# Performance work log

Hardware: AMD Instinct MI355X
Metric: run time of the kernel (lower is better)

Reference implementation:

```python
import jax, jax.numpy as jnp
import numpy as np

N = 100000
IN_F = 165
HID = 128
E = 1600000


def gcn_conv(x, W, b, src, dst, n):
    # PyG GCNConv: h = x @ W; add self-loops; symmetric norm D^-1/2 A D^-1/2; aggregate; + bias
    h = x @ W  # [n, out]
    src_sl = jnp.concatenate([src, jnp.arange(n)])
    dst_sl = jnp.concatenate([dst, jnp.arange(n)])
    deg = jax.ops.segment_sum(jnp.ones_like(src_sl, dtype=h.dtype), dst_sl, num_segments=n)
    dinv = jnp.where(deg > 0, jax.lax.rsqrt(deg), 0.0)
    norm = dinv[src_sl] * dinv[dst_sl]  # [e+n]
    msg = h[src_sl] * norm[:, None]
    out = jax.ops.segment_sum(msg, dst_sl, num_segments=n)
    return out + b


def setup_inputs() -> dict:
    key = jax.random.key(0)
    k = jax.random.split(key, 8)
    x = jax.random.normal(k[0], (N, IN_F), dtype=jnp.float32)
    edge_index = jax.random.randint(k[1], (2, E), 0, N)
    s1 = 1.0 / np.sqrt(IN_F)
    s2 = 1.0 / np.sqrt(HID)
    W1 = jax.random.uniform(k[2], (IN_F, HID), jnp.float32, -s1, s1)
    b1 = jnp.zeros((HID,), jnp.float32)
    W2 = jax.random.uniform(k[3], (HID, HID), jnp.float32, -s2, s2)
    b2 = jnp.zeros((HID,), jnp.float32)
    Wc = jax.random.uniform(k[4], (HID, 2), jnp.float32, -s2, s2)
    bc = jax.random.uniform(k[5], (2,), jnp.float32, -s2, s2)
    return {"x": x, "edge_index": edge_index, "W1": W1, "b1": b1,
            "W2": W2, "b2": b2, "Wc": Wc, "bc": bc}


def reference(x, edge_index, W1, b1, W2, b2, Wc, bc):
    src, dst = edge_index[0], edge_index[1]
    h = jax.nn.relu(gcn_conv(x, W1, b1, src, dst, N))
    # dropout inactive (eval mode)
    h = jax.nn.relu(gcn_conv(h, W2, b2, src, dst, N))
    return h @ Wc + bc
```

## Files before the change

kernel.cpp:

```cpp
#include <hip/hip_runtime.h>


typedef _Float16 half8 __attribute__((ext_vector_type(8)));
typedef float floatx4 __attribute__((ext_vector_type(4)));
typedef float f4u __attribute__((ext_vector_type(4), aligned(4)));

#define SLOT_C 64
#define BCAP 4608
#define NBKT 391
#define CHUNK 4096

__global__ __launch_bounds__(256) void multisplit_k(const int* __restrict__ src,
                                                    const int* __restrict__ dst, int e,
                                                    int* __restrict__ bcnt,
                                                    int2* __restrict__ edges2) {
  __shared__ int lhist[NBKT];
  __shared__ int lbase[NBKT];
  __shared__ int lcur[NBKT];
  int t = threadIdx.x;
  int e0 = blockIdx.x * CHUNK;
  int e1 = min(e0 + CHUNK, e);
  for (int b = t; b < NBKT; b += 256) { lhist[b] = 0; lcur[b] = 0; }
  __syncthreads();
  for (int i = e0 + t; i < e1; i += 256)
    atomicAdd(&lhist[dst[i] >> 8], 1);
  __syncthreads();
  for (int b = t; b < NBKT; b += 256) {
    int h = lhist[b];
    lbase[b] = h ? atomicAdd(&bcnt[b], h) : 0;
  }
  __syncthreads();
  for (int i = e0 + t; i < e1; i += 256) {
    int d = dst[i];
    int b = d >> 8;
    int p = lbase[b] + atomicAdd(&lcur[b], 1);
    if (p < BCAP) edges2[(size_t)b * BCAP + p] = make_int2(src[i], d);
  }
}

__global__ __launch_bounds__(256) void csr_from_bins_k(const int2* __restrict__ edges2,
                                                       const int* __restrict__ bcnt,
                                                       int* __restrict__ cnt_g,
                                                       int* __restrict__ csr,
                                                       float* __restrict__ dinv, int n) {
  __shared__ int lcnt[256];
  int b = blockIdx.x;
  int node0 = b << 8;
  int t = threadIdx.x;
  lcnt[t] = 0;
  __syncthreads();
  int ec = min(bcnt[b], BCAP);
  const int2* ebase = edges2 + (size_t)b * BCAP;
  for (int i = t; i < ec; i += 256) {
    int2 ed = ebase[i];
    int p = atomicAdd(&lcnt[ed.y - node0], 1);
    if (p < SLOT_C) csr[((size_t)ed.y << 6) + p] = ed.x;
  }
  __syncthreads();
  int node = node0 + t;
  if (node < n) {
    int c = lcnt[t];
    cnt_g[node] = c;
    dinv[node] = rsqrtf((float)(c + 1));
  }
}

__global__ void w_split_k(const float* __restrict__ W, int K, int Kpad,
                          _Float16* __restrict__ WhT, _Float16* __restrict__ WlT) {
  int idx = blockIdx.x * blockDim.x + threadIdx.x;
  if (idx >= 128 * Kpad) return;
  int c = idx / Kpad, k = idx - c * Kpad;
  float v = (k < K) ? W[(size_t)k * 128 + c] : 0.f;
  _Float16 h = (_Float16)v;
  WhT[idx] = h;
  WlT[idx] = (_Float16)(v - (float)h);
}

template <bool AHALF>
__global__ __launch_bounds__(256) void gemm_lds_k(const void* __restrict__ Av,
                                                  const _Float16* __restrict__ WhT,
                                                  const _Float16* __restrict__ WlT,
                                                  const float* __restrict__ rowscale,
                                                  _Float16* __restrict__ out,
                                                  int n, int K, int Kpad) {
  __shared__ alignas(16) float xt32[AHALF ? 1 : 128 * 36];
  __shared__ alignas(16) _Float16 xt16[AHALF ? 128 * 72 : 1];

  int t = threadIdx.x;
  int wave = t >> 6, lane = t & 63;
  int m = lane & 15, quad = lane >> 4;
  int row0 = blockIdx.x * 128;
  int rowbase = row0 + wave * 32;

  floatx4 acc[2][8];
#pragma unroll
  for (int tt = 0; tt < 2; ++tt)
#pragma unroll
    for (int j = 0; j < 8; ++j) acc[tt][j] = (floatx4){0.f, 0.f, 0.f, 0.f};

  int nslab = (K + 31) >> 5;
  for (int s = 0; s < nslab; ++s) {
    int kt = s << 5;

    if (!AHALF) {
#pragma unroll
      for (int p = 0; p < 4; ++p) {
        int idx = t + p * 256;
        int r = idx >> 3, cj = (idx & 7) << 2;
        int gr = row0 + r;
        float4 v = make_float4(0.f, 0.f, 0.f, 0.f);
        if (gr < n) {
          const float* arow = (const float*)Av + (size_t)gr * K + kt + cj;
          if (kt + 32 <= K) {
            f4u x = *(const f4u*)arow;
            v = make_float4(x.x, x.y, x.z, x.w);
          } else {
            int rem = K - kt - cj;
            if (rem > 0) v.x = arow[0];
            if (rem > 1) v.y = arow[1];
            if (rem > 2) v.z = arow[2];
            if (rem > 3) v.w = arow[3];
          }
        }
        *(float4*)&xt32[r * 36 + cj] = v;
      }
    } else {
      int r = t >> 1, cj = (t & 1) << 4;
      int gr = row0 + r;
      half8 v0 = (half8)(_Float16)0, v1 = (half8)(_Float16)0;
      if (gr < n) {
        const _Float16* arow = (const _Float16*)Av + (size_t)gr * K + kt + cj;
        v0 = *(const half8*)arow;
        v1 = *(const half8*)(arow + 8);
      }
      *(half8*)&xt16[r * 72 + cj] = v0;
      *(half8*)&xt16[r * 72 + cj + 8] = v1;
    }
    __syncthreads();

    half8 ah[2], al[2];
#pragma unroll
    for (int tt = 0; tt < 2; ++tt) {
      int rl = wave * 32 + tt * 16 + m;
      if (AHALF) {
        ah[tt] = *(const half8*)&xt16[rl * 72 + quad * 8];
      } else {
        f4u x0 = *(const f4u*)&xt32[rl * 36 + quad * 8];
        f4u x1 = *(const f4u*)&xt32[rl * 36 + quad * 8 + 4];
        float v[8] = {x0.x, x0.y, x0.z, x0.w, x1.x, x1.y, x1.z, x1.w};
#pragma unroll
        for (int j = 0; j < 8; ++j) {
          _Float16 h = (_Float16)v[j];
          ah[tt][j] = h;
          al[tt][j] = (_Float16)(v[j] - (float)h);
        }
      }
    }

    int k0 = kt + quad * 8;
#pragma unroll
    for (int g = 0; g < 2; ++g) {
      half8 wh[4], wl[4];
#pragma unroll
      for (int c = 0; c < 4; ++c) {
        size_t o = (size_t)((g * 4 + c) * 16 + m) * Kpad + k0;
        wh[c] = *(const half8*)(WhT + o);
        wl[c] = *(const half8*)(WlT + o);
      }
#pragma unroll
      for (int c = 0; c < 4; ++c) {
        int ct = g * 4 + c;
#pragma unroll
        for (int tt = 0; tt < 2; ++tt) {
          acc[tt][ct] = __builtin_amdgcn_mfma_f32_16x16x32_f16(ah[tt], wh[c], acc[tt][ct], 0, 0, 0);
          acc[tt][ct] = __builtin_amdgcn_mfma_f32_16x16x32_f16(ah[tt], wl[c], acc[tt][ct], 0, 0, 0);
          if (!AHALF)
            acc[tt][ct] = __builtin_amdgcn_mfma_f32_16x16x32_f16(al[tt], wh[c], acc[tt][ct], 0, 0, 0);
        }
      }
    }
    __syncthreads();
  }

#pragma unroll
  for (int tt = 0; tt < 2; ++tt) {
#pragma unroll
    for (int i = 0; i < 4; ++i) {
      int row = rowbase + tt * 16 + quad * 4 + i;
      if (row < n) {
        float di = rowscale ? rowscale[row] : 1.0f;
#pragma unroll
        for (int ct = 0; ct < 8; ++ct)
          out[(size_t)row * 128 + ct * 16 + m] = (_Float16)(acc[tt][ct][i] * di);
      }
    }
  }
}

template <bool CLS>
__global__ __launch_bounds__(256) void aggregate_k(const _Float16* __restrict__ g,
                                                   const int* __restrict__ cnt,
                                                   const int* __restrict__ csr,
                                                   const float* __restrict__ dinv,
                                                   const float* __restrict__ bias,
                                                   const float* __restrict__ Wc,
                                                   const float* __restrict__ bc,
                                                   _Float16* __restrict__ out16,
                                                   float* __restrict__ out32, int n) {
  int wave = threadIdx.x >> 6;
  int lane = threadIdx.x & 63;
  int i = blockIdx.x * 4 + wave;
  if (i >= n) return;
  int qtr = lane >> 4;
  int l16 = lane & 15;
  int f = l16 * 8;

  float acc[8];
#pragma unroll
  for (int j = 0; j < 8; ++j) acc[j] = 0.f;

  int deg = min(cnt[i], SLOT_C);
  size_t s0 = (size_t)i << 6;

  if (deg > 0) {
    int last = deg - 1;
    for (int eb = 0; eb < deg; eb += 16) {
#pragma unroll
      for (int k = 0; k < 4; ++k) {
        int ee = eb + 4 * k + qtr;
        float w = (ee <= last) ? 1.f : 0.f;
        int ec = (ee <= last) ? ee : last;
        int srow = csr[s0 + ec];
        half8 v = *(const half8*)&g[(size_t)srow * 128 + f];
#pragma unroll
        for (int j = 0; j < 8; ++j) acc[j] = fmaf(w, (float)v[j], acc[j]);
      }
    }
#pragma unroll
    for (int j = 0; j < 8; ++j) {
      acc[j] += __shfl_xor(acc[j], 16, 64);
      acc[j] += __shfl_xor(acc[j], 32, 64);
    }
  }

  half8 self = *(const half8*)&g[(size_t)i * 128 + f];
  float di = dinv[i];
  float4 b0 = *(const float4*)&bias[f];
  float4 b1 = *(const float4*)&bias[f + 4];
  float bv[8] = {b0.x, b0.y, b0.z, b0.w, b1.x, b1.y, b1.z, b1.w};
  float r[8];
#pragma unroll
  for (int j = 0; j < 8; ++j)
    r[j] = fmaxf((acc[j] + (float)self[j]) * di + bv[j], 0.f);

  if (!CLS) {
    if (qtr == 0) {
      half8 o;
#pragma unroll
      for (int j = 0; j < 8; ++j) o[j] = (_Float16)(r[j] * di);
      *(half8*)&out16[(size_t)i * 128 + f] = o;
    }
  } else {
    float c0v = 0.f, c1v = 0.f;
#pragma unroll
    for (int q = 0; q < 4; ++q) {
      float4 wv = *(const float4*)&Wc[f * 2 + q * 4];
      c0v += r[q * 2] * wv.x + r[q * 2 + 1] * wv.z;
      c1v += r[q * 2] * wv.y + r[q * 2 + 1] * wv.w;
    }
#pragma unroll
    for (int off = 8; off > 0; off >>= 1) {
      c0v += __shfl_down(c0v, off, 16);
      c1v += __shfl_down(c1v, off, 16);
    }
    if (lane == 0) {
      out32[(size_t)i * 2 + 0] = c0v + bc[0];
      out32[(size_t)i * 2 + 1] = c1v + bc[1];
    }
  }
}

extern "C" void kernel_launch(void* const* d_in, const int* in_sizes, int n_in,
                              void* d_out, int out_size, void* d_ws, size_t ws_size,
                              hipStream_t stream) {
  const float* x  = (const float*)d_in[0];
  const int*   ei = (const int*)d_in[1];
  const float* W1 = (const float*)d_in[2];
  const float* b1 = (const float*)d_in[3];
  const float* W2 = (const float*)d_in[4];
  const float* b2 = (const float*)d_in[5];
  const float* Wc = (const float*)d_in[6];
  const float* bc = (const float*)d_in[7];
  float* out = (float*)d_out;

  const int IN_F = 165;
  const int KP1 = 192;
  const int n = in_sizes[0] / IN_F;
  const int e = in_sizes[1] / 2;
  const int* src = ei;
  const int* dst = ei + e;

  char* ws = (char*)d_ws;
  size_t off = 0;
  auto alloc = [&](size_t bytes) -> void* {
    void* p = ws + off;
    off += (bytes + 255) & ~(size_t)255;
    return p;
  };
  _Float16* bufA = (_Float16*)alloc((size_t)n * 128 * 2);
  _Float16* bufB = (_Float16*)alloc((size_t)n * 128 * 2);
  int*   csr  = (int*)alloc((size_t)n * SLOT_C * 4);
  int2*  edges2 = (int2*)alloc((size_t)NBKT * BCAP * 8);
  int*   cnt  = (int*)alloc((size_t)n * 4);
  int*   bcnt = (int*)alloc((size_t)NBKT * 4);
  float* dinv = (float*)alloc((size_t)n * 4);
  _Float16* w1h = (_Float16*)alloc((size_t)128 * KP1 * 2);
  _Float16* w1l = (_Float16*)alloc((size_t)128 * KP1 * 2);
  _Float16* w2h = (_Float16*)alloc((size_t)128 * 128 * 2);
  _Float16* w2l = (_Float16*)alloc((size_t)128 * 128 * 2);

  hipMemsetAsync(bcnt, 0, (size_t)NBKT * 4, stream);

  const int tb = 256;
  w_split_k<<<(128 * KP1 + tb - 1) / tb, tb, 0, stream>>>(W1, IN_F, KP1, w1h, w1l);
  w_split_k<<<(128 * 128 + tb - 1) / tb, tb, 0, stream>>>(W2, 128, 128, w2h, w2l);

  multisplit_k<<<(e + CHUNK - 1) / CHUNK, 256, 0, stream>>>(src, dst, e, bcnt, edges2);
  csr_from_bins_k<<<NBKT, 256, 0, stream>>>(edges2, bcnt, cnt, csr, dinv, n);

  gemm_lds_k<false><<<(n + 127) / 128, 256, 0, stream>>>(x, w1h, w1l, dinv, bufA, n, IN_F, KP1);
  aggregate_k<false><<<(n + 3) / 4, 256, 0, stream>>>(bufA, cnt, csr, dinv, b1, nullptr, nullptr,
                                                      bufB, nullptr, n);
  gemm_lds_k<true><<<(n + 127) / 128, 256, 0, stream>>>(bufB, w2h, w2l, nullptr, bufA, n, 128, 128);
  aggregate_k<true><<<(n + 3) / 4, 256, 0, stream>>>(bufA, cnt, csr, dinv, b2, Wc, bc,
                                                     nullptr, out, n);
}
```

Baseline: 387.8 us.

## Load full-K row tile into LDS once and stream K slabs from it

Restructures the dense transform GEMM so each block stages a 64-row tile with the whole K dimension in LDS in one pass and a single barrier, instead of loading 32-wide K slabs with two barriers per slab. Each wave now handles 16 rows instead of 32, K and padded K become compile-time template parameters, and launch bounds request 3 blocks per CU. This cuts synchronisation and lets more blocks hide latency. In exchange, weight fragments are reused across fewer rows per wave, so global/L2 traffic for W roughly doubles, and the fp32 tile uses about 50KB of LDS.

```diff
diff --git a/kernel.cpp b/kernel.cpp
--- a/kernel.cpp
+++ b/kernel.cpp
@@ -76,123 +76,104 @@
   WlT[idx] = (_Float16)(v - (float)h);
 }
 
-template <bool AHALF>
-__global__ __launch_bounds__(256) void gemm_lds_k(const void* __restrict__ Av,
-                                                  const _Float16* __restrict__ WhT,
-                                                  const _Float16* __restrict__ WlT,
-                                                  const float* __restrict__ rowscale,
-                                                  _Float16* __restrict__ out,
-                                                  int n, int K, int Kpad) {
-  __shared__ alignas(16) float xt32[AHALF ? 1 : 128 * 36];
-  __shared__ alignas(16) _Float16 xt16[AHALF ? 128 * 72 : 1];
+template <bool AHALF, int KK, int KP>
+__global__ __launch_bounds__(256, 3) void gemm_stream_k(const void* __restrict__ Av,
+                                                        const _Float16* __restrict__ WhT,
+                                                        const _Float16* __restrict__ WlT,
+                                                        const float* __restrict__ rowscale,
+                                                        _Float16* __restrict__ out, int n) {
+  __shared__ alignas(16) float xt32[AHALF ? 1 : 64 * 196];
+  __shared__ alignas(16) _Float16 xt16[AHALF ? 64 * 136 : 1];
 
   int t = threadIdx.x;
   int wave = t >> 6, lane = t & 63;
   int m = lane & 15, quad = lane >> 4;
-  int row0 = blockIdx.x * 128;
-  int rowbase = row0 + wave * 32;
-
-  floatx4 acc[2][8];
-#pragma unroll
-  for (int tt = 0; tt < 2; ++tt)
-#pragma unroll
-    for (int j = 0; j < 8; ++j) acc[tt][j] = (floatx4){0.f, 0.f, 0.f, 0.f};
-
-  int nslab = (K + 31) >> 5;
-  for (int s = 0; s < nslab; ++s) {
-    int kt = s << 5;
-
-    if (!AHALF) {
-#pragma unroll
-      for (int p = 0; p < 4; ++p) {
-        int idx = t + p * 256;
-        int r = idx >> 3, cj = (idx & 7) << 2;
-        int gr = row0 + r;
-        float4 v = make_float4(0.f, 0.f, 0.f, 0.f);
-        if (gr < n) {
-          const float* arow = (const float*)Av + (size_t)gr * K + kt + cj;
-          if (kt + 32 <= K) {
-            f4u x = *(const f4u*)arow;
-            v = make_float4(x.x, x.y, x.z, x.w);
-          } else {
-            int rem = K - kt - cj;
-            if (rem > 0) v.x = arow[0];
-            if (rem > 1) v.y = arow[1];
-            if (rem > 2) v.z = arow[2];
-            if (rem > 3) v.w = arow[3];
-          }
+  int row0 = blockIdx.x * 64;
+
+  if (!AHALF) {
+    for (int idx = t; idx < 64 * 49; idx += 256) {
+      int r = idx / 49, c4 = idx - r * 49;
+      int c = c4 << 2;
+      int gr = row0 + r;
+      float4 v = make_float4(0.f, 0.f, 0.f, 0.f);
+      if (gr < n && c < KK) {
+        const float* arow = (const float*)Av + (size_t)gr * KK + c;
+        int rem = KK - c;
+        if (rem >= 4) {
+          f4u x = *(const f4u*)arow;
+          v = make_float4(x.x, x.y, x.z, x.w);
+        } else {
+          if (rem > 0) v.x = arow[0];
+          if (rem > 1) v.y = arow[1];
+          if (rem > 2) v.z = arow[2];
         }
-        *(float4*)&xt32[r * 36 + cj] = v;
-      }
+      }
+      *(float4*)&xt32[r * 196 + c] = v;
+    }
+  } else {
+    for (int idx = t; idx < 64 * 16; idx += 256) {
+      int r = idx >> 4, c = (idx & 15) << 3;
+      int gr = row0 + r;
+      half8 v = (half8)(_Float16)0;
+      if (gr < n) v = *(const half8*)((const _Float16*)Av + (size_t)gr * KK + c);
+      *(half8*)&xt16[r * 136 + c] = v;
+    }
+  }
+  __syncthreads();
+
+  floatx4 acc[8];
+#pragma unroll
+  for (int j = 0; j < 8; ++j) acc[j] = (floatx4){0.f, 0.f, 0.f, 0.f};
+
+  int rl = wave * 16 + m;
+  constexpr int NSLAB = KP >> 5;
+#pragma unroll 2
+  for (int s = 0; s < NSLAB; ++s) {
+    int k0 = (s << 5) + quad * 8;
+
+    half8 ah, al;
+    if (AHALF) {
+      ah = *(const half8*)&xt16[rl * 136 + k0];
     } else {
-      int r = t >> 1, cj = (t & 1) << 4;
-      int gr = row0 + r;
-      half8 v0 = (half8)(_Float16)0, v1 = (half8)(_Float16)0;
-      if (gr < n) {
-        const _Float16* arow = (const _Float16*)Av + (size_t)gr * K + kt + cj;
-        v0 = *(const half8*)arow;
-        v1 = *(const half8*)(arow + 8);
-      }
-      *(half8*)&xt16[r * 72 + cj] = v0;
-      *(half8*)&xt16[r * 72 + cj + 8] = v1;
-    }
-    __syncthreads();
-
-    half8 ah[2], al[2];
-#pragma unroll
-    for (int tt = 0; tt < 2; ++tt) {
-      int rl = wave * 32 + tt * 16 + m;
-      if (AHALF) {
-        ah[tt] = *(const half8*)&xt16[rl * 72 + quad * 8];
-      } else {
-        f4u x0 = *(const f4u*)&xt32[rl * 36 + quad * 8];
-        f4u x1 = *(const f4u*)&xt32[rl * 36 + quad * 8 + 4];
-        float v[8] = {x0.x, x0.y, x0.z, x0.w, x1.x, x1.y, x1.z, x1.w};
-#pragma unroll
-        for (int j = 0; j < 8; ++j) {
-          _Float16 h = (_Float16)v[j];
-          ah[tt][j] = h;
-          al[tt][j] = (_Float16)(v[j] - (float)h);
-        }
-      }
-    }
-
-    int k0 = kt + quad * 8;
+      f4u x0 = *(const f4u*)&xt32[rl * 196 + k0];
+      f4u x1 = *(const f4u*)&xt32[rl * 196 + k0 + 4];
+      float v[8] = {x0.x, x0.y, x0.z, x0.w, x1.x, x1.y, x1.z, x1.w};
+#pragma unroll
+      for (int j = 0; j < 8; ++j) {
+        _Float16 h = (_Float16)v[j];
+        ah[j] = h;
+        al[j] = (_Float16)(v[j] - (float)h);
+      }
+    }
+
 #pragma unroll
     for (int g = 0; g < 2; ++g) {
       half8 wh[4], wl[4];
 #pragma unroll
       for (int c = 0; c < 4; ++c) {
-        size_t o = (size_t)((g * 4 + c) * 16 + m) * Kpad + k0;
+        size_t o = (size_t)((g * 4 + c) * 16 + m) * KP + k0;
         wh[c] = *(const half8*)(WhT + o);
         wl[c] = *(const half8*)(WlT + o);
       }
 #pragma unroll
       for (int c = 0; c < 4; ++c) {
         int ct = g * 4 + c;
-#pragma unroll
-        for (int tt = 0; tt < 2; ++tt) {
-          acc[tt][ct] = __builtin_amdgcn_mfma_f32_16x16x32_f16(ah[tt], wh[c], acc[tt][ct], 0, 0, 0);
-          acc[tt][ct] = __builtin_amdgcn_mfma_f32_16x16x32_f16(ah[tt], wl[c], acc[tt][ct], 0, 0, 0);
-          if (!AHALF)
-            acc[tt][ct] = __builtin_amdgcn_mfma_f32_16x16x32_f16(al[tt], wh[c], acc[tt][ct], 0, 0, 0);
-        }
-      }
-    }
-    __syncthreads();
-  }
-
-#pragma unroll
-  for (int tt = 0; tt < 2; ++tt) {
-#pragma unroll
-    for (int i = 0; i < 4; ++i) {
-      int row = rowbase + tt * 16 + quad * 4 + i;
-      if (row < n) {
-        float di = rowscale ? rowscale[row] : 1.0f;
-#pragma unroll
-        for (int ct = 0; ct < 8; ++ct)
-          out[(size_t)row * 128 + ct * 16 + m] = (_Float16)(acc[tt][ct][i] * di);
-      }
+        acc[ct] = __builtin_amdgcn_mfma_f32_16x16x32_f16(ah, wh[c], acc[ct], 0, 0, 0);
+        acc[ct] = __builtin_amdgcn_mfma_f32_16x16x32_f16(ah, wl[c], acc[ct], 0, 0, 0);
+        if (!AHALF)
+          acc[ct] = __builtin_amdgcn_mfma_f32_16x16x32_f16(al, wh[c], acc[ct], 0, 0, 0);
+      }
+    }
+  }
+
+#pragma unroll
+  for (int i = 0; i < 4; ++i) {
+    int row = row0 + wave * 16 + quad * 4 + i;
+    if (row < n) {
+      float di = rowscale ? rowscale[row] : 1.0f;
+#pragma unroll
+      for (int ct = 0; ct < 8; ++ct)
+        out[(size_t)row * 128 + ct * 16 + m] = (_Float16)(acc[ct][i] * di);
     }
   }
 }
@@ -328,10 +309,10 @@
   multisplit_k<<<(e + CHUNK - 1) / CHUNK, 256, 0, stream>>>(src, dst, e, bcnt, edges2);
   csr_from_bins_k<<<NBKT, 256, 0, stream>>>(edges2, bcnt, cnt, csr, dinv, n);
 
-  gemm_lds_k<false><<<(n + 127) / 128, 256, 0, stream>>>(x, w1h, w1l, dinv, bufA, n, IN_F, KP1);
+  gemm_stream_k<false, 165, 192><<<(n + 63) / 64, 256, 0, stream>>>(x, w1h, w1l, dinv, bufA, n);
   aggregate_k<false><<<(n + 3) / 4, 256, 0, stream>>>(bufA, cnt, csr, dinv, b1, nullptr, nullptr,
                                                       bufB, nullptr, n);
-  gemm_lds_k<true><<<(n + 127) / 128, 256, 0, stream>>>(bufB, w2h, w2l, nullptr, bufA, n, 128, 128);
+  gemm_stream_k<true, 128, 128><<<(n + 63) / 64, 256, 0, stream>>>(bufB, w2h, w2l, nullptr, bufA, n);
   aggregate_k<true><<<(n + 3) / 4, 256, 0, stream>>>(bufA, cnt, csr, dinv, b2, Wc, bc,
                                                      nullptr, out, n);
 }
```

Measured after the change: 435.1 us. 1.12x slower.
